# Performance work log

Hardware: AMD Instinct MI355X
Metric: run time of the kernel (lower is better)

## Reference

```python
import jax, jax.numpy as jnp
import numpy as np

B, T, D = 32, 256, 384
MAX_LEN = 2048

def setup_inputs() -> dict:
    key = jax.random.key(0)
    k1, k2 = jax.random.split(key)
    x = jax.random.normal(k1, (B, T, D), dtype=jnp.float32)
    duration = jax.random.randint(k2, (B, T), 0, 8, dtype=jnp.int64)
    return {"x": x, "duration": duration, "max_len": MAX_LEN}


def reference(x, duration, max_len):
    # x: [B, T, D] phoneme features; duration: [B, T] int repeat counts.
    # Fused expand-by-duration + pad via cumulative offsets + gather.
    csum = jnp.cumsum(duration, axis=1)                       # [B, T]
    mel_len = csum[:, -1]                                     # [B]
    frames = jnp.arange(max_len)                              # [max_len]
    # frame j belongs to phoneme i where csum[i-1] <= j < csum[i]
    idx = jax.vmap(lambda c: jnp.searchsorted(c, frames, side='right'))(csum)  # [B, max_len]
    valid = frames[None, :] < mel_len[:, None]                # [B, max_len]
    idx = jnp.clip(idx, 0, x.shape[1] - 1)
    out = jnp.take_along_axis(x, idx[:, :, None], axis=1)     # [B, max_len, D]
    out = jnp.where(valid[:, :, None], out, 0.0)
    return out, mel_len
```

## Files before the change

### kernel.cpp

```cpp
#include <hip/hip_runtime.h>


#define BB 32
#define TT 256
#define DD 384
#define MAXLEN 2048
#define D4 (DD / 4)
#define FPB 8
#define TILES (MAXLEN / FPB)

__global__ __launch_bounds__(256) void scan_kernel(const int* __restrict__ duration,
                                                   int* __restrict__ csum,
                                                   float* __restrict__ mel_out) {
    __shared__ int s[TT];
    const int b = blockIdx.x;
    const int t = threadIdx.x;
    s[t] = duration[b * TT + t];
    __syncthreads();
    for (int off = 1; off < TT; off <<= 1) {
        int cur = s[t];
        int add = (t >= off) ? s[t - off] : 0;
        __syncthreads();
        s[t] = cur + add;
        __syncthreads();
    }
    csum[b * TT + t] = s[t];
    if (t == TT - 1) {
        mel_out[b] = (float)s[t];
    }
}

__global__ __launch_bounds__(256) void expand_kernel(const float* __restrict__ x,
                                                     const int* __restrict__ csum,
                                                     float* __restrict__ out) {
    __shared__ int s_csum[TT];
    __shared__ int s_idx[FPB];

    const int bid = blockIdx.x;
    const int b = bid >> 8;
    const int tile = bid & (TILES - 1);
    const int tid = threadIdx.x;

    s_csum[tid] = csum[b * TT + tid];
    __syncthreads();

    if (tid < FPB) {
        const int f = tile * FPB + tid;
        const int mel = s_csum[TT - 1];
        int idx = -1;
        if (f < mel) {
            int lo = 0, hi = TT;
            while (lo < hi) {
                int mid = (lo + hi) >> 1;
                if (s_csum[mid] > f) hi = mid; else lo = mid + 1;
            }
            idx = lo;
        }
        s_idx[tid] = idx;
    }
    __syncthreads();

    const float4* __restrict__ x4 = (const float4*)(x + (size_t)b * TT * DD);
    float4* __restrict__ o4 = (float4*)(out + ((size_t)b * MAXLEN + (size_t)tile * FPB) * DD);

    #pragma unroll
    for (int i = 0; i < (FPB * D4) / 256; ++i) {
        const int g = i * 256 + tid;
        const int fl = g / D4;
        const int vv = g - fl * D4;
        const int idx = s_idx[fl];
        float4 val;
        if (idx >= 0) {
            val = x4[idx * D4 + vv];
        } else {
            val = make_float4(0.f, 0.f, 0.f, 0.f);
        }
        o4[g] = val;
    }
}

extern "C" void kernel_launch(void* const* d_in, const int* in_sizes, int n_in,
                              void* d_out, int out_size, void* d_ws, size_t ws_size,
                              hipStream_t stream) {
    const float* x = (const float*)d_in[0];
    const int* duration = (const int*)d_in[1];

    float* out = (float*)d_out;
    float* mel_out = out + (size_t)BB * MAXLEN * DD;
    int* csum = (int*)d_ws;

    scan_kernel<<<BB, TT, 0, stream>>>(duration, csum, mel_out);
    expand_kernel<<<BB * TILES, 256, 0, stream>>>(x, csum, out);
}
```

Before: 120.8 us.

## Precompute frame-to-phoneme index table in scan kernel, enlarge tiles, fast-path padding

The scan kernel now scatters each phoneme index into a per-frame index table, with -1 for padding frames. The expand kernel then reads indices directly instead of loading the full cumsum and binary searching. Tiles grow from 8 to 32 frames per block, and tiles that start in padding write zeros without touching x. This trades per-block search and cumsum loads for a small serial scatter in the scan kernel.

Result: slower. 126.6 us (+4.8%).

```diff
diff --git a/kernel.cpp b/kernel.cpp
--- a/kernel.cpp
+++ b/kernel.cpp
@@ -6,16 +6,17 @@
 #define DD 384
 #define MAXLEN 2048
 #define D4 (DD / 4)
-#define FPB 8
+#define FPB 32
 #define TILES (MAXLEN / FPB)
 
-__global__ __launch_bounds__(256) void scan_kernel(const int* __restrict__ duration,
-                                                   int* __restrict__ csum,
-                                                   float* __restrict__ mel_out) {
+__global__ __launch_bounds__(256) void scan_scatter_kernel(const int* __restrict__ duration,
+                                                           int* __restrict__ idx_tbl,
+                                                           float* __restrict__ mel_out) {
     __shared__ int s[TT];
     const int b = blockIdx.x;
     const int t = threadIdx.x;
-    s[t] = duration[b * TT + t];
+    const int d = duration[b * TT + t];
+    s[t] = d;
     __syncthreads();
     for (int off = 1; off < TT; off <<= 1) {
         int cur = s[t];
@@ -24,44 +25,43 @@
         s[t] = cur + add;
         __syncthreads();
     }
-    csum[b * TT + t] = s[t];
+    const int end = s[t];
+    const int mel = s[TT - 1];
+    int* __restrict__ row = idx_tbl + b * MAXLEN;
+    for (int f = end - d; f < end; ++f) row[f] = t;
+    for (int f = mel + t; f < MAXLEN; f += TT) row[f] = -1;
     if (t == TT - 1) {
-        mel_out[b] = (float)s[t];
+        mel_out[b] = (float)end;
     }
 }
 
 __global__ __launch_bounds__(256) void expand_kernel(const float* __restrict__ x,
-                                                     const int* __restrict__ csum,
+                                                     const int* __restrict__ idx_tbl,
                                                      float* __restrict__ out) {
-    __shared__ int s_csum[TT];
     __shared__ int s_idx[FPB];
 
     const int bid = blockIdx.x;
-    const int b = bid >> 8;
+    const int b = bid >> 6;
     const int tile = bid & (TILES - 1);
     const int tid = threadIdx.x;
 
-    s_csum[tid] = csum[b * TT + tid];
-    __syncthreads();
-
     if (tid < FPB) {
-        const int f = tile * FPB + tid;
-        const int mel = s_csum[TT - 1];
-        int idx = -1;
-        if (f < mel) {
-            int lo = 0, hi = TT;
-            while (lo < hi) {
-                int mid = (lo + hi) >> 1;
-                if (s_csum[mid] > f) hi = mid; else lo = mid + 1;
-            }
-            idx = lo;
-        }
-        s_idx[tid] = idx;
+        s_idx[tid] = idx_tbl[b * MAXLEN + tile * FPB + tid];
     }
     __syncthreads();
 
+    float4* __restrict__ o4 = (float4*)(out + ((size_t)b * MAXLEN + (size_t)tile * FPB) * DD);
+
+    if (s_idx[0] < 0) {
+        const float4 z = make_float4(0.f, 0.f, 0.f, 0.f);
+        #pragma unroll
+        for (int i = 0; i < (FPB * D4) / 256; ++i) {
+            o4[i * 256 + tid] = z;
+        }
+        return;
+    }
+
     const float4* __restrict__ x4 = (const float4*)(x + (size_t)b * TT * DD);
-    float4* __restrict__ o4 = (float4*)(out + ((size_t)b * MAXLEN + (size_t)tile * FPB) * DD);
 
     #pragma unroll
     for (int i = 0; i < (FPB * D4) / 256; ++i) {
@@ -69,11 +69,9 @@
         const int fl = g / D4;
         const int vv = g - fl * D4;
         const int idx = s_idx[fl];
-        float4 val;
+        float4 val = make_float4(0.f, 0.f, 0.f, 0.f);
         if (idx >= 0) {
-            val = x4[idx * D4 + vv];
-        } else {
-            val = make_float4(0.f, 0.f, 0.f, 0.f);
+            val = x4[(size_t)idx * D4 + vv];
         }
         o4[g] = val;
     }
@@ -87,8 +85,8 @@
 
     float* out = (float*)d_out;
     float* mel_out = out + (size_t)BB * MAXLEN * DD;
-    int* csum = (int*)d_ws;
+    int* idx_tbl = (int*)d_ws;
 
-    scan_kernel<<<BB, TT, 0, stream>>>(duration, csum, mel_out);
-    expand_kernel<<<BB * TILES, 256, 0, stream>>>(x, csum, out);
+    scan_scatter_kernel<<<BB, TT, 0, stream>>>(duration, idx_tbl, mel_out);
+    expand_kernel<<<BB * TILES, 256, 0, stream>>>(x, idx_tbl, out);
 }
```

## Fuse duration scan into expand kernel with wave-shuffle scan and nontemporal stores

Applied to the files above, without the earlier changes.

Removes the separate scan kernel and its workspace round-trip: every expand block recomputes the per-batch prefix sum itself, using wave-level shuffles plus a small cross-wave combine. Tiles grow from 8 to 32 frames per block, block IDs are remapped so consecutive blocks spread across XCDs, and fully padded tiles take an early path that only writes zeros. Output writes use nontemporal stores to avoid polluting cache. The trade-off is redundant scan work in every block and fewer, larger blocks.

New measurement: 127.0 us. 5.1% more time.

```diff
diff --git a/kernel.cpp b/kernel.cpp
--- a/kernel.cpp
+++ b/kernel.cpp
@@ -6,47 +6,49 @@
 #define DD 384
 #define MAXLEN 2048
 #define D4 (DD / 4)
-#define FPB 8
+#define FPB 32
 #define TILES (MAXLEN / FPB)
+#define NBLK (BB * TILES)
 
-__global__ __launch_bounds__(256) void scan_kernel(const int* __restrict__ duration,
-                                                   int* __restrict__ csum,
-                                                   float* __restrict__ mel_out) {
-    __shared__ int s[TT];
-    const int b = blockIdx.x;
-    const int t = threadIdx.x;
-    s[t] = duration[b * TT + t];
-    __syncthreads();
-    for (int off = 1; off < TT; off <<= 1) {
-        int cur = s[t];
-        int add = (t >= off) ? s[t - off] : 0;
-        __syncthreads();
-        s[t] = cur + add;
-        __syncthreads();
-    }
-    csum[b * TT + t] = s[t];
-    if (t == TT - 1) {
-        mel_out[b] = (float)s[t];
-    }
-}
+typedef float vf4 __attribute__((ext_vector_type(4)));
 
-__global__ __launch_bounds__(256) void expand_kernel(const float* __restrict__ x,
-                                                     const int* __restrict__ csum,
-                                                     float* __restrict__ out) {
+__global__ __launch_bounds__(256) void fused_kernel(const float* __restrict__ x,
+                                                    const int* __restrict__ duration,
+                                                    float* __restrict__ out,
+                                                    float* __restrict__ mel_out) {
     __shared__ int s_csum[TT];
+    __shared__ int s_wsum[4];
     __shared__ int s_idx[FPB];
 
-    const int bid = blockIdx.x;
-    const int b = bid >> 8;
-    const int tile = bid & (TILES - 1);
+    const int l = (blockIdx.x & 7) * (NBLK / 8) + (blockIdx.x >> 3);
+    const int b = l >> 6;
+    const int tile = l & (TILES - 1);
     const int tid = threadIdx.x;
+    const int lane = tid & 63;
+    const int wave = tid >> 6;
 
-    s_csum[tid] = csum[b * TT + tid];
+    int v = duration[b * TT + tid];
+    #pragma unroll
+    for (int off = 1; off < 64; off <<= 1) {
+        int n = __shfl_up(v, off, 64);
+        if (lane >= off) v += n;
+    }
+    if (lane == 63) s_wsum[wave] = v;
     __syncthreads();
+    int pre = 0;
+    #pragma unroll
+    for (int w = 0; w < 3; ++w) pre += (w < wave) ? s_wsum[w] : 0;
+    const int inc = v + pre;
+    s_csum[tid] = inc;
+    if (tile == 0 && tid == TT - 1) {
+        mel_out[b] = (float)inc;
+    }
+    __syncthreads();
+
+    const int mel = s_csum[TT - 1];
 
     if (tid < FPB) {
         const int f = tile * FPB + tid;
-        const int mel = s_csum[TT - 1];
         int idx = -1;
         if (f < mel) {
             int lo = 0, hi = TT;
@@ -60,8 +62,18 @@
     }
     __syncthreads();
 
-    const float4* __restrict__ x4 = (const float4*)(x + (size_t)b * TT * DD);
-    float4* __restrict__ o4 = (float4*)(out + ((size_t)b * MAXLEN + (size_t)tile * FPB) * DD);
+    vf4* __restrict__ o4 = (vf4*)(out + ((size_t)b * MAXLEN + (size_t)tile * FPB) * DD);
+
+    if (s_idx[0] < 0) {
+        const vf4 z = {0.f, 0.f, 0.f, 0.f};
+        #pragma unroll
+        for (int i = 0; i < (FPB * D4) / 256; ++i) {
+            __builtin_nontemporal_store(z, o4 + i * 256 + tid);
+        }
+        return;
+    }
+
+    const vf4* __restrict__ x4 = (const vf4*)(x + (size_t)b * TT * DD);
 
     #pragma unroll
     for (int i = 0; i < (FPB * D4) / 256; ++i) {
@@ -69,13 +81,11 @@
         const int fl = g / D4;
         const int vv = g - fl * D4;
         const int idx = s_idx[fl];
-        float4 val;
+        vf4 val = {0.f, 0.f, 0.f, 0.f};
         if (idx >= 0) {
-            val = x4[idx * D4 + vv];
-        } else {
-            val = make_float4(0.f, 0.f, 0.f, 0.f);
+            val = x4[(size_t)idx * D4 + vv];
         }
-        o4[g] = val;
+        __builtin_nontemporal_store(val, o4 + g);
     }
 }
 
@@ -87,8 +97,7 @@
 
     float* out = (float*)d_out;
     float* mel_out = out + (size_t)BB * MAXLEN * DD;
-    int* csum = (int*)d_ws;
+    (void)d_ws; (void)ws_size;
 
-    scan_kernel<<<BB, TT, 0, stream>>>(duration, csum, mel_out);
-    expand_kernel<<<BB * TILES, 256, 0, stream>>>(x, csum, out);
+    fused_kernel<<<NBLK, TT, 0, stream>>>(x, duration, out, mel_out);
 }
```
